# Kernel optimization log

Measured on AMD Instinct MI355X. Metric: run time of the kernel, lower is better.

## Reference

```python
import jax, jax.numpy as jnp
import numpy as np
from math import sqrt

B, Q, S, D, H = 2, 2048, 2048, 1024, 16
ADIM = D // H
IEPS = 1e-32


def setup_inputs() -> dict:
    key = jax.random.key(0)
    ks = jax.random.split(key, 7)
    sc = 0.02
    return {
        "iQ": jax.random.normal(ks[0], (B, Q, D), jnp.float32),
        "iK": jax.random.normal(ks[1], (B, S, D), jnp.float32),
        "mask": jax.random.randint(ks[2], (B, Q, S), 0, 2) > 0,
        "Wq": jax.random.normal(ks[3], (D, D), jnp.float32) * sc,
        "Wkv": jax.random.normal(ks[4], (2 * D, D), jnp.float32) * sc,
        "Wo": jax.random.normal(ks[5], (D, D), jnp.float32) * sc,
        "nbias": jnp.zeros((1,), jnp.float32),
    }


def sparse_norm(scores, nbias):
    # ReLU(x + b)^2 normalized along last axis (SparseNormer)
    t = jax.nn.relu(scores + nbias[0])
    t = t * t
    return t / (t.sum(-1, keepdims=True) + IEPS)


def reference(iQ, iK, mask, Wq, Wkv, Wo, nbias):
    b, q, _ = iQ.shape
    s = iK.shape[1]
    # projections (no bias)
    rq = (iQ @ Wq.T).reshape(b, q, H, ADIM)            # bqhd
    kv = (iK @ Wkv.T).reshape(b, s, 2, H, ADIM)
    rk, rv = kv[:, :, 0], kv[:, :, 1]                  # bshd each
    scores = jnp.einsum("bqhd,bshd->bhqs", rq, rk) / sqrt(ADIM)
    scores = jnp.where(mask[:, None, :, :], jnp.float32(-1e32), scores)
    attn = sparse_norm(scores, nbias)
    o = jnp.einsum("bhqs,bshd->bqhd", attn, rv).reshape(b, q, H * ADIM)
    return o @ Wo.T
```

## Files before the change

kernel.cpp:

```cpp
#include <hip/hip_runtime.h>

#define Bb 2
#define Qq 2048
#define Ss 2048
#define Dd 1024
#define Hh 16
#define AD 64
#define KK 1024

typedef __attribute__((ext_vector_type(8))) short bf16x8;
typedef __attribute__((ext_vector_type(4))) short bf16x4;
typedef __attribute__((ext_vector_type(4))) float f32x4;
typedef unsigned short u16;
typedef unsigned int u32;
typedef unsigned long long u64;

__device__ __forceinline__ u16 f2bf(float f) {
  union { float f; u32 u; } v; v.f = f;
  u32 r = v.u + 0x7fffu + ((v.u >> 16) & 1u);
  return (u16)(r >> 16);
}

__device__ __forceinline__ void gld16(const u16* g, u16* l) {
  __builtin_amdgcn_global_load_lds(
      (const __attribute__((address_space(1))) unsigned int*)g,
      (__attribute__((address_space(3))) unsigned int*)l, 16, 0, 0);
}

__global__ __launch_bounds__(256) void cast_all_k(const float* __restrict__ iQ,
                                                  const float* __restrict__ iK,
                                                  const float* __restrict__ Wq,
                                                  const float* __restrict__ Wkv,
                                                  const float* __restrict__ Wo,
                                                  const int* __restrict__ mask,
                                                  u16* __restrict__ Qb, u16* __restrict__ Kb,
                                                  u16* __restrict__ Wqb, u16* __restrict__ Wkvb,
                                                  u16* __restrict__ Wob,
                                                  u64* __restrict__ mb64) {
  int i = blockIdx.x * 256 + threadIdx.x;
  if (i < 3145728) {
    const float* src; u16* dst; int off;
    if (i < 1048576)      { src = iQ;  dst = Qb;   off = 0; }
    else if (i < 2097152) { src = iK;  dst = Kb;   off = 1048576; }
    else if (i < 2359296) { src = Wq;  dst = Wqb;  off = 2097152; }
    else if (i < 2883584) { src = Wkv; dst = Wkvb; off = 2359296; }
    else                  { src = Wo;  dst = Wob;  off = 2883584; }
    int j = i - off;
    float4 v = ((const float4*)src)[j];
    ushort4 o;
    o.x = f2bf(v.x); o.y = f2bf(v.y); o.z = f2bf(v.z); o.w = f2bf(v.w);
    ((ushort4*)dst)[j] = o;
  } else {
    int flat = i - 3145728;
    int st = flat & 31;
    int q  = (flat >> 5) & 2047;
    int b  = flat >> 16;
    const int4* src = (const int4*)(mask + ((size_t)(b * Qq + q)) * Ss + st * 64);
    u64 bits = 0;
#pragma unroll
    for (int c = 0; c < 16; c++) {
      int4 v = src[c];
      bits |= (u64)(v.x != 0) << (c * 4 + 0);
      bits |= (u64)(v.y != 0) << (c * 4 + 1);
      bits |= (u64)(v.z != 0) << (c * 4 + 2);
      bits |= (u64)(v.w != 0) << (c * 4 + 3);
    }
    mb64[flat] = bits;
  }
}

__global__ __launch_bounds__(256, 3) void proj_k(const u16* __restrict__ Qb,
                                                 const u16* __restrict__ Kb,
                                                 const u16* __restrict__ Wqb,
                                                 const u16* __restrict__ Wkvb,
                                                 u16* __restrict__ RQ,
                                                 u16* __restrict__ Kc,
                                                 u16* __restrict__ VT) {
  __shared__ char LB[34816];
  u16* As = (u16*)LB;
  u16* Ws = (u16*)(LB + 16384);
  const int tid = threadIdx.x;
  const int lane = tid & 63, wave = tid >> 6;
  const int qr = lane & 15, quad = lane >> 4;
  const int qs = qr & 7;
  const int bid = blockIdx.x;
  const bool isQ = bid < 256;
  const int b2 = isQ ? bid : bid - 256;
  const int m0 = (b2 & 31) * 128;
  const int n0 = (b2 >> 5) * 128;
  const u16* A = isQ ? Qb : Kb;
  const u16* W = isQ ? Wqb : Wkvb;
  const int wm = (wave >> 1) * 64, wn = (wave & 1) * 64;

  const int sr = tid >> 3, sc = tid & 7;
  const u16 *aP[4], *wP[4];
  u16 *aL[4], *wL[4];
#pragma unroll
  for (int is = 0; is < 4; is++) {
    int row = is * 32 + sr;
    int goff = (sc ^ (row & 7)) * 8;
    aP[is] = A + (size_t)(m0 + row) * KK + goff;
    wP[is] = W + (size_t)(n0 + row) * KK + goff;
    aL[is] = As + row * 64 + sc * 8;
    wL[is] = Ws + row * 64 + sc * 8;
  }

  f32x4 acc[4][4] = {};

  for (int k0 = 0; k0 < KK; k0 += 64) {
#pragma unroll
    for (int is = 0; is < 4; is++) gld16(aP[is] + k0, aL[is]);
#pragma unroll
    for (int is = 0; is < 4; is++) gld16(wP[is] + k0, wL[is]);
    __syncthreads();
#pragma unroll
    for (int kk = 0; kk < 2; kk++) {
      bf16x8 af[4], bw[4];
      int ch = ((kk * 4 + quad) ^ qs) * 8;
#pragma unroll
      for (int i = 0; i < 4; i++)
        af[i] = *(const bf16x8*)(As + (wm + i * 16 + qr) * 64 + ch);
#pragma unroll
      for (int j = 0; j < 4; j++)
        bw[j] = *(const bf16x8*)(Ws + (wn + j * 16 + qr) * 64 + ch);
#pragma unroll
      for (int i = 0; i < 4; i++)
#pragma unroll
        for (int j = 0; j < 4; j++)
          acc[i][j] = __builtin_amdgcn_mfma_f32_16x16x32_bf16(af[i], bw[j], acc[i][j], 0, 0, 0);
    }
    __syncthreads();
  }

  if (isQ) {
#pragma unroll
    for (int i = 0; i < 4; i++)
#pragma unroll
      for (int j = 0; j < 4; j++)
#pragma unroll
        for (int r = 0; r < 4; r++) {
          int row = m0 + wm + i * 16 + quad * 4 + r;
          int col = n0 + wn + j * 16 + qr;
          RQ[(size_t)row * 1024 + col] = f2bf(acc[i][j][r] * 0.125f);
        }
  } else if (n0 < 1024) {
#pragma unroll
    for (int i = 0; i < 4; i++)
#pragma unroll
      for (int j = 0; j < 4; j++)
#pragma unroll
        for (int r = 0; r < 4; r++) {
          int row = m0 + wm + i * 16 + quad * 4 + r;
          int col = n0 + wn + j * 16 + qr;
          Kc[(size_t)row * 1024 + col] = f2bf(acc[i][j][r]);
        }
  } else {
    u16* Ttp = (u16*)LB + (wn >> 6) * (64 * 136);
#pragma unroll
    for (int i = 0; i < 4; i++)
#pragma unroll
      for (int j = 0; j < 4; j++)
#pragma unroll
        for (int r = 0; r < 4; r++) {
          int srow = wm + i * 16 + quad * 4 + r;
          int d    = j * 16 + qr;
          Ttp[d * 136 + srow] = f2bf(acc[i][j][r]);
        }
    __syncthreads();
    const int h0 = (n0 - 1024) >> 6;
    const int bb = m0 >> 11, sbase = m0 & 2047;
    const u16* LB16 = (const u16*)LB;
#pragma unroll
    for (int ic = 0; ic < 8; ic++) {
      int flat = ic * 256 + tid;
      int hd = flat >> 10, d = (flat >> 4) & 63, ch = flat & 15;
      *(int4*)(VT + (((size_t)(bb * Hh + h0 + hd)) * AD + d) * Ss + sbase + ch * 8) =
          *(const int4*)(LB16 + hd * (64 * 136) + d * 136 + ch * 8);
    }
  }
}

__global__ __launch_bounds__(256, 3) void oproj_k(const u16* __restrict__ A,
                                                  const u16* __restrict__ W,
                                                  float* __restrict__ C) {
  __shared__ u16 As[128 * 64];
  __shared__ u16 Ws[128 * 64];
  const int tid = threadIdx.x;
  const int lane = tid & 63, wave = tid >> 6;
  const int qr = lane & 15, quad = lane >> 4;
  const int qs = qr & 7;
  const int m0 = (blockIdx.x & 31) * 128;
  const int n0 = (blockIdx.x >> 5) * 128;
  const int wm = (wave >> 1) * 64, wn = (wave & 1) * 64;
  const int sr = tid >> 3, sc = tid & 7;
  const u16 *aP[4], *wP[4];
  u16 *aL[4], *wL[4];
#pragma unroll
  for (int is = 0; is < 4; is++) {
    int row = is * 32 + sr;
    int goff = (sc ^ (row & 7)) * 8;
    aP[is] = A + (size_t)(m0 + row) * KK + goff;
    wP[is] = W + (size_t)(n0 + row) * KK + goff;
    aL[is] = As + row * 64 + sc * 8;
    wL[is] = Ws + row * 64 + sc * 8;
  }
  f32x4 acc[4][4] = {};
  for (int k0 = 0; k0 < KK; k0 += 64) {
#pragma unroll
    for (int is = 0; is < 4; is++) gld16(aP[is] + k0, aL[is]);
#pragma unroll
    for (int is = 0; is < 4; is++) gld16(wP[is] + k0, wL[is]);
    __syncthreads();
#pragma unroll
    for (int kk = 0; kk < 2; kk++) {
      bf16x8 af[4], bw[4];
      int ch = ((kk * 4 + quad) ^ qs) * 8;
#pragma unroll
      for (int i = 0; i < 4; i++)
        af[i] = *(const bf16x8*)(As + (wm + i * 16 + qr) * 64 + ch);
#pragma unroll
      for (int j = 0; j < 4; j++)
        bw[j] = *(const bf16x8*)(Ws + (wn + j * 16 + qr) * 64 + ch);
#pragma unroll
      for (int i = 0; i < 4; i++)
#pragma unroll
        for (int j = 0; j < 4; j++)
          acc[i][j] = __builtin_amdgcn_mfma_f32_16x16x32_bf16(af[i], bw[j], acc[i][j], 0, 0, 0);
    }
    __syncthreads();
  }
#pragma unroll
  for (int i = 0; i < 4; i++)
#pragma unroll
    for (int j = 0; j < 4; j++)
#pragma unroll
      for (int r = 0; r < 4; r++) {
        int row = m0 + wm + i * 16 + quad * 4 + r;
        int col = n0 + wn + j * 16 + qr;
        C[(size_t)row * 1024 + col] = acc[i][j][r];
      }
}

__global__ __launch_bounds__(512, 4) void attn_k(const u16* __restrict__ RQ,
                                                 const u16* __restrict__ Kc,
                                                 const u16* __restrict__ VT,
                                                 const u64* __restrict__ mb64,
                                                 const float* __restrict__ nbias,
                                                 u16* __restrict__ O) {
  __shared__ char LB[65536];
  u16* Ks  = (u16*)LB;
  u16* Vts = (u16*)(LB + 32768);
  f32x4* Xch = (f32x4*)LB;

  const int tid = threadIdx.x, lane = tid & 63, w = tid >> 6;
  const int qh = w >> 1, sh = w & 1;
  const int qr = lane & 15, quad = lane >> 4;
  const int quad4 = quad * 4, qs = qr & 7;
  const int q0 = blockIdx.x * 128, h = blockIdx.y, b = blockIdx.z;
  const u16* rqb = RQ + ((size_t)(b * Qq + q0)) * Dd + h * AD;
  const u16* kb  = Kc + ((size_t)b * Ss) * 1024 + h * AD;
  const u16* vtb = VT + ((size_t)(b * Hh + h)) * AD * Ss;
  const u64* mbase = mb64 + ((size_t)(b * Qq + q0)) * 32;
  const float nb = nbias[0];

  bf16x8 bq[2][2];
#pragma unroll
  for (int j = 0; j < 2; j++)
#pragma unroll
    for (int kk = 0; kk < 2; kk++)
      bq[j][kk] = *(const bf16x8*)(rqb + (size_t)(qh * 32 + j * 16 + qr) * Dd +
                                   kk * 32 + quad * 8);

  const u16 *kP[4], *vP[4];
  u16 *kL[4], *vL[4];
  {
    const int r8 = tid >> 3, c8 = tid & 7;
#pragma unroll
    for (int is = 0; is < 4; is++) {
      int row = is * 64 + r8;
      kP[is] = kb + (size_t)row * 1024 + ((c8 ^ (row & 7)) * 8);
      kL[is] = Ks + row * 64 + c8 * 8;
    }
    const int r32 = tid >> 5, c32 = tid & 31;
#pragma unroll
    for (int is = 0; is < 4; is++) {
      int row = is * 16 + r32;
      vP[is] = vtb + (size_t)row * Ss + ((c32 ^ (row & 7)) * 8);
      vL[is] = Vts + row * 256 + c32 * 8;
    }
  }

  const bf16x4 vones = { (short)0x3F80, (short)0x3F80, (short)0x3F80, (short)0x3F80 };
  f32x4 acc[2][4] = {};
  f32x4 accd[2] = {};

  const u16* kfr = Ks + (sh * 128 + qr) * 64;
  const u16* kfr0 = kfr + ((quad ^ qs) * 8);
  const u16* kfr1 = kfr + (((quad + 4) ^ qs) * 8);

  for (int t = 0; t < 8; t++) {
    __syncthreads();
#pragma unroll
    for (int is = 0; is < 4; is++) gld16(kP[is] + (size_t)t * 262144, kL[is]);
#pragma unroll
    for (int is = 0; is < 4; is++) gld16(vP[is] + t * 256, vL[is]);
    u64 mw[2][2];
#pragma unroll
    for (int j = 0; j < 2; j++) {
      const u64* mp = mbase + (size_t)(qh * 32 + j * 16 + qr) * 32 + t * 4 + sh * 2;
      mw[j][0] = mp[0];
      mw[j][1] = mp[1];
    }
    __syncthreads();

#pragma unroll
    for (int mi = 0; mi < 8; mi++) {
      bf16x8 ak0 = *(const bf16x8*)(kfr0 + mi * 1024);
      bf16x8 ak1 = *(const bf16x8*)(kfr1 + mi * 1024);
      f32x4 asc0 = { nb, nb, nb, nb };
      f32x4 asc1 = { nb, nb, nb, nb };
      asc0 = __builtin_amdgcn_mfma_f32_16x16x32_bf16(ak0, bq[0][0], asc0, 0, 0, 0);
      asc0 = __builtin_amdgcn_mfma_f32_16x16x32_bf16(ak1, bq[0][1], asc0, 0, 0, 0);
      asc1 = __builtin_amdgcn_mfma_f32_16x16x32_bf16(ak0, bq[1][0], asc1, 0, 0, 0);
      asc1 = __builtin_amdgcn_mfma_f32_16x16x32_bf16(ak1, bq[1][1], asc1, 0, 0, 0);

      union { u32 w2[2]; bf16x4 v; } pk[2];
#pragma unroll
      for (int j = 0; j < 2; j++) {
        f32x4 asc = j ? asc1 : asc0;
        u32 mm = (u32)(mw[j][mi >> 2] >> ((mi & 3) * 16 + quad4)) & 0xFu;
        u32 th[4];
#pragma unroll
        for (int r = 0; r < 4; r++) {
          float tt = fmaxf(asc[r], 0.f);
          tt = tt * tt;
          if ((mm >> r) & 1) tt = 0.f;
          union { float f; u32 u; } cv; cv.f = tt;
          th[r] = cv.u;
        }
        pk[j].w2[0] = __builtin_amdgcn_perm(th[1], th[0], 0x07060302u);
        pk[j].w2[1] = __builtin_amdgcn_perm(th[3], th[2], 0x07060302u);
        accd[j] = __builtin_amdgcn_mfma_f32_16x16x16bf16_1k(pk[j].v, vones, accd[j], 0, 0, 0);
      }
      int g = ((sh * 32 + mi * 4 + quad) ^ (qs << 1)) * 4;
#pragma unroll
      for (int nn = 0; nn < 4; nn++) {
        bf16x4 bv = *(const bf16x4*)(Vts + (nn * 16 + qr) * 256 + g);
        acc[0][nn] = __builtin_amdgcn_mfma_f32_16x16x16bf16_1k(pk[0].v, bv, acc[0][nn], 0, 0, 0);
        acc[1][nn] = __builtin_amdgcn_mfma_f32_16x16x16bf16_1k(pk[1].v, bv, acc[1][nn], 0, 0, 0);
      }
    }
  }

  __syncthreads();
  if (sh == 1) {
#pragma unroll
    for (int j = 0; j < 2; j++) {
#pragma unroll
      for (int nn = 0; nn < 4; nn++)
        Xch[qh * 640 + (j * 4 + nn) * 64 + lane] = acc[j][nn];
      Xch[qh * 640 + (8 + j) * 64 + lane] = accd[j];
    }
  }
  __syncthreads();
  if (sh == 0) {
    u16* ob = O + ((size_t)(b * Qq + q0)) * Dd + h * AD;
#pragma unroll
    for (int j = 0; j < 2; j++) {
      f32x4 dpart = Xch[qh * 640 + (8 + j) * 64 + lane];
      float rc[4];
#pragma unroll
      for (int r = 0; r < 4; r++)
        rc[r] = 1.f / (accd[j][r] + dpart[r] + 1e-32f);
#pragma unroll
      for (int nn = 0; nn < 4; nn++) {
        f32x4 p4 = Xch[qh * 640 + (j * 4 + nn) * 64 + lane];
#pragma unroll
        for (int r = 0; r < 4; r++) {
          int ql = qh * 32 + j * 16 + quad * 4 + r;
          ob[(size_t)ql * Dd + nn * 16 + qr] = f2bf((acc[j][nn][r] + p4[r]) * rc[r]);
        }
      }
    }
  }
}

extern "C" void kernel_launch(void* const* d_in, const int* in_sizes, int n_in,
                              void* d_out, int out_size, void* d_ws, size_t ws_size,
                              hipStream_t stream) {
  const float* iQ   = (const float*)d_in[0];
  const float* iK   = (const float*)d_in[1];
  const int*   mask = (const int*)d_in[2];
  const float* Wq   = (const float*)d_in[3];
  const float* Wkv  = (const float*)d_in[4];
  const float* Wo   = (const float*)d_in[5];
  const float* nb   = (const float*)d_in[6];

  char* ws = (char*)d_ws;
  u16* Qb   = (u16*)(ws + (size_t)0);
  u16* Kb   = (u16*)(ws + ((size_t)8  << 20));
  u16* Wqb  = (u16*)(ws + ((size_t)16 << 20));
  u16* Wkvb = (u16*)(ws + ((size_t)18 << 20));
  u16* Wob  = (u16*)(ws + ((size_t)22 << 20));
  u16* RQ   = (u16*)(ws + ((size_t)24 << 20));
  u16* Kc   = (u16*)(ws + ((size_t)32 << 20));
  u16* Obuf = (u16*)(ws + ((size_t)48 << 20));
  u16* VT   = (u16*)(ws + ((size_t)56 << 20));
  u64* MB   = (u64*)(ws + ((size_t)64 << 20));

  cast_all_k<<<12800, 256, 0, stream>>>(iQ, iK, Wq, Wkv, Wo, mask,
                                        Qb, Kb, Wqb, Wkvb, Wob, MB);

  proj_k<<<768, 256, 0, stream>>>(Qb, Kb, Wqb, Wkvb, RQ, Kc, VT);

  attn_k<<<dim3(16, 16, 2), 512, 0, stream>>>(RQ, Kc, VT, MB, nb, Obuf);

  oproj_k<<<256, 256, 0, stream>>>(Obuf, Wob, (float*)d_out);
}
```

Before: 244.5 us.

## Use 16x16x32 MFMA for PV, halve oproj tile, shrink proj transpose LDS

The attention PV product now packs two 16-key score tiles into one bf16x8 operand, so the 16x16x32 MFMA replaces pairs of 16x16x16 MFMAs for both the value accumulation and the row-sum. Key rows and V-tile chunk indices are remapped so each lane's K fragments line up with the new 8-element packing. The output projection tile shrinks from 128x128 to 128x64, doubling the grid to 512 blocks and raising occupancy. The projection kernel's V transpose now stages one head at a time through a smaller LDS buffer, which costs an extra barrier pair.

```diff
diff --git a/kernel.cpp b/kernel.cpp
--- a/kernel.cpp
+++ b/kernel.cpp
@@ -76,7 +76,7 @@
                                                  u16* __restrict__ RQ,
                                                  u16* __restrict__ Kc,
                                                  u16* __restrict__ VT) {
-  __shared__ char LB[34816];
+  __shared__ char LB[32768];
   u16* As = (u16*)LB;
   u16* Ws = (u16*)(LB + 16384);
   const int tid = threadIdx.x;
@@ -155,76 +155,86 @@
           Kc[(size_t)row * 1024 + col] = f2bf(acc[i][j][r]);
         }
   } else {
-    u16* Ttp = (u16*)LB + (wn >> 6) * (64 * 136);
-#pragma unroll
-    for (int i = 0; i < 4; i++)
-#pragma unroll
-      for (int j = 0; j < 4; j++)
-#pragma unroll
-        for (int r = 0; r < 4; r++) {
-          int srow = wm + i * 16 + quad * 4 + r;
-          int d    = j * 16 + qr;
-          Ttp[d * 136 + srow] = f2bf(acc[i][j][r]);
-        }
-    __syncthreads();
     const int h0 = (n0 - 1024) >> 6;
     const int bb = m0 >> 11, sbase = m0 & 2047;
-    const u16* LB16 = (const u16*)LB;
-#pragma unroll
-    for (int ic = 0; ic < 8; ic++) {
-      int flat = ic * 256 + tid;
-      int hd = flat >> 10, d = (flat >> 4) & 63, ch = flat & 15;
-      *(int4*)(VT + (((size_t)(bb * Hh + h0 + hd)) * AD + d) * Ss + sbase + ch * 8) =
-          *(const int4*)(LB16 + hd * (64 * 136) + d * 136 + ch * 8);
-    }
-  }
-}
-
-__global__ __launch_bounds__(256, 3) void oproj_k(const u16* __restrict__ A,
+    u16* Tt = (u16*)LB;
+#pragma unroll
+    for (int hd = 0; hd < 2; hd++) {
+      __syncthreads();
+      if ((wave & 1) == hd) {
+#pragma unroll
+        for (int i = 0; i < 4; i++)
+#pragma unroll
+          for (int j = 0; j < 4; j++)
+#pragma unroll
+            for (int r = 0; r < 4; r++) {
+              int srow = wm + i * 16 + quad * 4 + r;
+              int d    = j * 16 + qr;
+              Tt[d * 136 + srow] = f2bf(acc[i][j][r]);
+            }
+      }
+      __syncthreads();
+#pragma unroll
+      for (int ic = 0; ic < 4; ic++) {
+        int flat = ic * 256 + tid;
+        int d = flat >> 4, ch = flat & 15;
+        *(int4*)(VT + (((size_t)(bb * Hh + h0 + hd)) * AD + d) * Ss + sbase + ch * 8) =
+            *(const int4*)(Tt + d * 136 + ch * 8);
+      }
+    }
+  }
+}
+
+__global__ __launch_bounds__(256, 4) void oproj_k(const u16* __restrict__ A,
                                                   const u16* __restrict__ W,
                                                   float* __restrict__ C) {
   __shared__ u16 As[128 * 64];
-  __shared__ u16 Ws[128 * 64];
+  __shared__ u16 Ws[64 * 64];
   const int tid = threadIdx.x;
   const int lane = tid & 63, wave = tid >> 6;
   const int qr = lane & 15, quad = lane >> 4;
   const int qs = qr & 7;
   const int m0 = (blockIdx.x & 31) * 128;
-  const int n0 = (blockIdx.x >> 5) * 128;
-  const int wm = (wave >> 1) * 64, wn = (wave & 1) * 64;
+  const int n0 = (blockIdx.x >> 5) * 64;
+  const int wm = (wave >> 1) * 64, wn = (wave & 1) * 32;
   const int sr = tid >> 3, sc = tid & 7;
-  const u16 *aP[4], *wP[4];
-  u16 *aL[4], *wL[4];
+  const u16 *aP[4], *wP[2];
+  u16 *aL[4], *wL[2];
 #pragma unroll
   for (int is = 0; is < 4; is++) {
     int row = is * 32 + sr;
     int goff = (sc ^ (row & 7)) * 8;
     aP[is] = A + (size_t)(m0 + row) * KK + goff;
+    aL[is] = As + row * 64 + sc * 8;
+  }
+#pragma unroll
+  for (int is = 0; is < 2; is++) {
+    int row = is * 32 + sr;
+    int goff = (sc ^ (row & 7)) * 8;
     wP[is] = W + (size_t)(n0 + row) * KK + goff;
-    aL[is] = As + row * 64 + sc * 8;
     wL[is] = Ws + row * 64 + sc * 8;
   }
-  f32x4 acc[4][4] = {};
+  f32x4 acc[4][2] = {};
   for (int k0 = 0; k0 < KK; k0 += 64) {
 #pragma unroll
     for (int is = 0; is < 4; is++) gld16(aP[is] + k0, aL[is]);
 #pragma unroll
-    for (int is = 0; is < 4; is++) gld16(wP[is] + k0, wL[is]);
+    for (int is = 0; is < 2; is++) gld16(wP[is] + k0, wL[is]);
     __syncthreads();
 #pragma unroll
     for (int kk = 0; kk < 2; kk++) {
-      bf16x8 af[4], bw[4];
+      bf16x8 af[4], bw[2];
       int ch = ((kk * 4 + quad) ^ qs) * 8;
 #pragma unroll
       for (int i = 0; i < 4; i++)
         af[i] = *(const bf16x8*)(As + (wm + i * 16 + qr) * 64 + ch);
 #pragma unroll
-      for (int j = 0; j < 4; j++)
+      for (int j = 0; j < 2; j++)
         bw[j] = *(const bf16x8*)(Ws + (wn + j * 16 + qr) * 64 + ch);
 #pragma unroll
       for (int i = 0; i < 4; i++)
 #pragma unroll
-        for (int j = 0; j < 4; j++)
+        for (int j = 0; j < 2; j++)
           acc[i][j] = __builtin_amdgcn_mfma_f32_16x16x32_bf16(af[i], bw[j], acc[i][j], 0, 0, 0);
     }
     __syncthreads();
@@ -232,7 +242,7 @@
 #pragma unroll
   for (int i = 0; i < 4; i++)
 #pragma unroll
-    for (int j = 0; j < 4; j++)
+    for (int j = 0; j < 2; j++)
 #pragma unroll
       for (int r = 0; r < 4; r++) {
         int row = m0 + wm + i * 16 + quad * 4 + r;
@@ -255,7 +265,7 @@
   const int tid = threadIdx.x, lane = tid & 63, w = tid >> 6;
   const int qh = w >> 1, sh = w & 1;
   const int qr = lane & 15, quad = lane >> 4;
-  const int quad4 = quad * 4, qs = qr & 7;
+  const int qs = qr & 7;
   const int q0 = blockIdx.x * 128, h = blockIdx.y, b = blockIdx.z;
   const u16* rqb = RQ + ((size_t)(b * Qq + q0)) * Dd + h * AD;
   const u16* kb  = Kc + ((size_t)b * Ss) * 1024 + h * AD;
@@ -290,13 +300,15 @@
     }
   }
 
-  const bf16x4 vones = { (short)0x3F80, (short)0x3F80, (short)0x3F80, (short)0x3F80 };
+  const bf16x8 vones8 = { (short)0x3F80, (short)0x3F80, (short)0x3F80, (short)0x3F80,
+                          (short)0x3F80, (short)0x3F80, (short)0x3F80, (short)0x3F80 };
   f32x4 acc[2][4] = {};
   f32x4 accd[2] = {};
 
-  const u16* kfr = Ks + (sh * 128 + qr) * 64;
-  const u16* kfr0 = kfr + ((quad ^ qs) * 8);
-  const u16* kfr1 = kfr + (((quad + 4) ^ qs) * 8);
+  const int keyE = qr & 3, keyF = keyE + 4;
+  const u16* krowE = Ks + (sh * 128 + ((qr >> 2) << 3) + (qr & 3)) * 64;
+  const int ofsE0 = (quad ^ keyE) * 8,       ofsE1 = ((4 + quad) ^ keyE) * 8;
+  const int ofsF0 = 256 + (quad ^ keyF) * 8, ofsF1 = 256 + ((4 + quad) ^ keyF) * 8;
 
   for (int t = 0; t < 8; t++) {
     __syncthreads();
@@ -314,40 +326,50 @@
     __syncthreads();
 
 #pragma unroll
-    for (int mi = 0; mi < 8; mi++) {
-      bf16x8 ak0 = *(const bf16x8*)(kfr0 + mi * 1024);
-      bf16x8 ak1 = *(const bf16x8*)(kfr1 + mi * 1024);
-      f32x4 asc0 = { nb, nb, nb, nb };
-      f32x4 asc1 = { nb, nb, nb, nb };
-      asc0 = __builtin_amdgcn_mfma_f32_16x16x32_bf16(ak0, bq[0][0], asc0, 0, 0, 0);
-      asc0 = __builtin_amdgcn_mfma_f32_16x16x32_bf16(ak1, bq[0][1], asc0, 0, 0, 0);
-      asc1 = __builtin_amdgcn_mfma_f32_16x16x32_bf16(ak0, bq[1][0], asc1, 0, 0, 0);
-      asc1 = __builtin_amdgcn_mfma_f32_16x16x32_bf16(ak1, bq[1][1], asc1, 0, 0, 0);
-
-      union { u32 w2[2]; bf16x4 v; } pk[2];
+    for (int p = 0; p < 4; p++) {
+      const u16* kpb = krowE + p * 2048;
+      bf16x8 akE0 = *(const bf16x8*)(kpb + ofsE0);
+      bf16x8 akE1 = *(const bf16x8*)(kpb + ofsE1);
+      bf16x8 akF0 = *(const bf16x8*)(kpb + ofsF0);
+      bf16x8 akF1 = *(const bf16x8*)(kpb + ofsF1);
+      f32x4 aE[2] = { { nb, nb, nb, nb }, { nb, nb, nb, nb } };
+      f32x4 aF[2] = { { nb, nb, nb, nb }, { nb, nb, nb, nb } };
 #pragma unroll
       for (int j = 0; j < 2; j++) {
-        f32x4 asc = j ? asc1 : asc0;
-        u32 mm = (u32)(mw[j][mi >> 2] >> ((mi & 3) * 16 + quad4)) & 0xFu;
-        u32 th[4];
+        aE[j] = __builtin_amdgcn_mfma_f32_16x16x32_bf16(akE0, bq[j][0], aE[j], 0, 0, 0);
+        aE[j] = __builtin_amdgcn_mfma_f32_16x16x32_bf16(akE1, bq[j][1], aE[j], 0, 0, 0);
+        aF[j] = __builtin_amdgcn_mfma_f32_16x16x32_bf16(akF0, bq[j][0], aF[j], 0, 0, 0);
+        aF[j] = __builtin_amdgcn_mfma_f32_16x16x32_bf16(akF1, bq[j][1], aF[j], 0, 0, 0);
+      }
+
+      union { u32 w4[4]; bf16x8 v; } pk8[2];
+#pragma unroll
+      for (int j = 0; j < 2; j++) {
+        u32 bsh = (u32)((p & 1) * 32 + quad * 8);
+        u32 mmE = (u32)(mw[j][p >> 1] >> bsh) & 0xFu;
+        u32 mmF = (u32)(mw[j][p >> 1] >> (bsh + 4)) & 0xFu;
+        u32 thE[4], thF[4];
 #pragma unroll
         for (int r = 0; r < 4; r++) {
-          float tt = fmaxf(asc[r], 0.f);
-          tt = tt * tt;
-          if ((mm >> r) & 1) tt = 0.f;
-          union { float f; u32 u; } cv; cv.f = tt;
-          th[r] = cv.u;
+          float tE = fmaxf(aE[j][r], 0.f); tE = tE * tE;
+          if ((mmE >> r) & 1) tE = 0.f;
+          float tF = fmaxf(aF[j][r], 0.f); tF = tF * tF;
+          if ((mmF >> r) & 1) tF = 0.f;
+          union { float f; u32 u; } cE; cE.f = tE; thE[r] = cE.u;
+          union { float f; u32 u; } cF; cF.f = tF; thF[r] = cF.u;
         }
-        pk[j].w2[0] = __builtin_amdgcn_perm(th[1], th[0], 0x07060302u);
-        pk[j].w2[1] = __builtin_amdgcn_perm(th[3], th[2], 0x07060302u);
-        accd[j] = __builtin_amdgcn_mfma_f32_16x16x16bf16_1k(pk[j].v, vones, accd[j], 0, 0, 0);
-      }
-      int g = ((sh * 32 + mi * 4 + quad) ^ (qs << 1)) * 4;
+        pk8[j].w4[0] = __builtin_amdgcn_perm(thE[1], thE[0], 0x07060302u);
+        pk8[j].w4[1] = __builtin_amdgcn_perm(thE[3], thE[2], 0x07060302u);
+        pk8[j].w4[2] = __builtin_amdgcn_perm(thF[1], thF[0], 0x07060302u);
+        pk8[j].w4[3] = __builtin_amdgcn_perm(thF[3], thF[2], 0x07060302u);
+        accd[j] = __builtin_amdgcn_mfma_f32_16x16x32_bf16(pk8[j].v, vones8, accd[j], 0, 0, 0);
+      }
+      int cidx = sh * 16 + p * 4 + quad;
 #pragma unroll
       for (int nn = 0; nn < 4; nn++) {
-        bf16x4 bv = *(const bf16x4*)(Vts + (nn * 16 + qr) * 256 + g);
-        acc[0][nn] = __builtin_amdgcn_mfma_f32_16x16x16bf16_1k(pk[0].v, bv, acc[0][nn], 0, 0, 0);
-        acc[1][nn] = __builtin_amdgcn_mfma_f32_16x16x16bf16_1k(pk[1].v, bv, acc[1][nn], 0, 0, 0);
+        bf16x8 bv = *(const bf16x8*)(Vts + (nn * 16 + qr) * 256 + (cidx ^ qs) * 8);
+        acc[0][nn] = __builtin_amdgcn_mfma_f32_16x16x32_bf16(pk8[0].v, bv, acc[0][nn], 0, 0, 0);
+        acc[1][nn] = __builtin_amdgcn_mfma_f32_16x16x32_bf16(pk8[1].v, bv, acc[1][nn], 0, 0, 0);
       }
     }
   }
@@ -415,5 +437,5 @@
 
   attn_k<<<dim3(16, 16, 2), 512, 0, stream>>>(RQ, Kc, VT, MB, nb, Obuf);
 
-  oproj_k<<<256, 256, 0, stream>>>(Obuf, Wob, (float*)d_out);
-}
+  oproj_k<<<512, 256, 0, stream>>>(Obuf, Wob, (float*)d_out);
+}
```

New measurement: 248.4 us. About the same (+1.6%).
